# Kernel optimization log

Measured on AMD Instinct MI355X. Metric: run time of the kernel, lower is better.

The kernel has to match this reference:

```python
import jax, jax.numpy as jnp
import numpy as np

N = 50000      # nodes
E = 800000     # edges (before self-loops)
DIN = 2        # dim_input
DEMB = 128     # dim_embedding
H = 8          # n_heads
DV = 16        # dim_values (H*DV == DEMB)
DH = 512       # dim_hidden
L = 2          # n_att_layers
K = 10         # APPNP steps
ALPHA = 0.1
EPS = 1e-5     # BatchNorm eps
NEG_SLOPE = 0.2  # GAT leaky_relu slope


def setup_inputs() -> dict:
    key = jax.random.key(0)
    ks = jax.random.split(key, 16)
    s = 0.05
    inp = {}
    inp["x"] = jax.random.normal(ks[0], (N, DIN), jnp.float32)
    inp["J"] = jax.random.uniform(ks[1], (N, 1), jnp.float32)
    inp["edge_index"] = jax.random.randint(ks[2], (2, E), 0, N, jnp.int32)
    # Lin1: Linear(dim_input+1, dim_embedding)
    inp["lin0_w"] = jax.random.normal(ks[3], (DIN + 1, DEMB), jnp.float32) * s
    inp["lin0_b"] = jnp.zeros((DEMB,), jnp.float32)
    # Per attention layer (stacked over L):
    inp["gat_w"]   = jax.random.normal(ks[4], (L, DEMB, H * DV), jnp.float32) * s
    inp["att_src"] = jax.random.normal(ks[5], (L, H, DV), jnp.float32) * s
    inp["att_dst"] = jax.random.normal(ks[6], (L, H, DV), jnp.float32) * s
    inp["lin1_w"]  = jax.random.normal(ks[7], (L, DV, DEMB), jnp.float32) * s
    inp["bn1_g"]   = jnp.ones((L, DEMB), jnp.float32)
    inp["bn1_b"]   = jnp.zeros((L, DEMB), jnp.float32)
    inp["lin2_w"]  = jax.random.normal(ks[8], (L, DEMB, DH), jnp.float32) * s
    inp["lin2_b"]  = jnp.zeros((L, DH), jnp.float32)
    inp["lin3_w"]  = jax.random.normal(ks[9], (L, DH, DEMB), jnp.float32) * s
    inp["lin3_b"]  = jnp.zeros((L, DEMB), jnp.float32)
    inp["bn2_g"]   = jnp.ones((L, DEMB), jnp.float32)
    inp["bn2_b"]   = jnp.zeros((L, DEMB), jnp.float32)
    return inp


def _bn(z, g, b):
    # BatchNorm1d over nodes, training-mode batch statistics (biased var)
    mu = z.mean(0)
    var = jnp.mean((z - mu) ** 2, axis=0)
    return g * (z - mu) * jax.lax.rsqrt(var + EPS) + b


def reference(x, J, edge_index, lin0_w, lin0_b, gat_w, att_src, att_dst,
              lin1_w, bn1_g, bn1_b, lin2_w, lin2_b, lin3_w, lin3_b,
              bn2_g, bn2_b):
    # add self-loops (PyG GATConv and APPNP defaults)
    loop = jnp.arange(N, dtype=edge_index.dtype)
    src = jnp.concatenate([edge_index[0], loop])  # message source j
    dst = jnp.concatenate([edge_index[1], loop])  # message target i

    h = jnp.concatenate([x, J], axis=1) @ lin0_w + lin0_b  # [N, DEMB]

    for l in range(L):
        # ---- GATConv ----
        xl = (h @ gat_w[l]).reshape(N, H, DV)                # [N,H,DV]
        a_s = (xl * att_src[l]).sum(-1)                      # [N,H]
        a_d = (xl * att_dst[l]).sum(-1)                      # [N,H]
        e = jax.nn.leaky_relu(a_s[src] + a_d[dst], NEG_SLOPE)  # [E',H]
        e = e - jax.ops.segment_max(e, dst, num_segments=N)[dst]
        ee = jnp.exp(e)
        alpha = ee / jax.ops.segment_sum(ee, dst, num_segments=N)[dst]
        msg = xl[src] * alpha[:, :, None]                    # [E',H,DV]
        gat_out = jax.ops.segment_sum(msg, dst, num_segments=N)  # [N,H,DV]
        # lin1 per head then sum over heads
        hsum = jnp.einsum('nhc,cd->nd', gat_out, lin1_w[l])  # [N,DEMB]
        h1 = _bn(h + hsum, bn1_g[l], bn1_b[l])
        h2 = jax.nn.relu(h1 @ lin2_w[l] + lin2_b[l]) @ lin3_w[l] + lin3_b[l]
        h = _bn(h2 + h1, bn2_g[l], bn2_b[l])

    # ---- APPNP: K steps of (1-a)*Ahat h + a*h0, Ahat = D^-1/2 (A+I) D^-1/2 ----
    deg = jax.ops.segment_sum(jnp.ones_like(dst, jnp.float32), dst, num_segments=N)
    dinv = jax.lax.rsqrt(jnp.maximum(deg, 1.0))  # self-loops guarantee deg>=1
    norm = (dinv[src] * dinv[dst])[:, None]      # [E',1]
    h0 = h

    def step(hk, _):
        agg = jax.ops.segment_sum(norm * hk[src], dst, num_segments=N)
        return (1.0 - ALPHA) * agg + ALPHA * h0, None

    h, _ = jax.lax.scan(step, h, None, length=K)
    return jnp.concatenate([h, J], axis=1)  # [N, DEMB+1]
```

## Files before the change

kernel.cpp:

```cpp
#include <hip/hip_runtime.h>

#define NN 50000
#define NN1 50001
#define NP 50048
#define NMT64 782
#define NE 800000
#define EP (NE + NN)
#define EPP_MAX (EP + 7 * NN + 64)
#define DEMB 128
#define DHID 512
#define NB_SCAN 196

typedef unsigned short ushort_t;
typedef __attribute__((ext_vector_type(8))) short short8_t;
typedef __attribute__((ext_vector_type(4))) float float4_t;

__device__ __forceinline__ float bf2f(ushort_t u) {
    return __uint_as_float(((unsigned int)u) << 16);
}
__device__ __forceinline__ ushort_t f2bf(float f) {
    unsigned int x = __float_as_uint(f);
    x += 0x7fffu + ((x >> 16) & 1u);
    return (ushort_t)(x >> 16);
}
__device__ __forceinline__ float lo16(unsigned int w) { return __uint_as_float(w << 16); }
__device__ __forceinline__ float hi16(unsigned int w) { return __uint_as_float(w & 0xffff0000u); }
__device__ __forceinline__ unsigned int pack2(float a, float b) {
    return (unsigned int)f2bf(a) | ((unsigned int)f2bf(b) << 16);
}
__device__ __forceinline__ void gl_lds16(const ushort_t* g, ushort_t* l) {
    __builtin_amdgcn_global_load_lds(
        (const __attribute__((address_space(1))) void*)g,
        (__attribute__((address_space(3))) void*)l, 16, 0, 0);
}
static inline int cdiv(int a, int b) { return (a + b - 1) / b; }

__global__ void k_detect(const unsigned int* __restrict__ Jw, int* __restrict__ flag) {
    if (threadIdx.x != 0 || blockIdx.x != 0) return;
    int votes = 0;
    for (int i = 0; i < 8; ++i) {
        unsigned int w = Jw[i];
        unsigned int ex = (w >> 23) & 0xFFu;
        if ((w >> 31) == 0u && ex >= 100u && ex <= 126u) votes++;
    }
    *flag = (votes >= 6) ? 1 : 0;
}

struct CvtArgs {
    const void* src[16];
    float* dst[16];
    int n[16];
};
__global__ void k_cvt_all(CvtArgs a, const int* __restrict__ flag) {
    int which = blockIdx.y;
    int i = blockIdx.x * 256 + threadIdx.x;
    if (i >= a.n[which]) return;
    float v;
    if (*flag) v = ((const float*)a.src[which])[i];
    else       v = bf2f(((const ushort_t*)a.src[which])[i]);
    a.dst[which][i] = v;
}

struct TrArgs {
    const float* src[6];
    ushort_t* dst[6];
    int K[6];
    int Nc[6];
    int perm[6];
};
__global__ void k_tr_all(TrArgs a) {
    int which = blockIdx.y;
    int idx = blockIdx.x * 256 + threadIdx.x;
    int K = a.K[which], Nc = a.Nc[which];
    if (idx >= K * Nc) return;
    int k = idx / Nc, n = idx - k * Nc;
    int kd = k;
    if (a.perm[which]) {
        int kk = k & 63;
        kd = (k & ~63) | ((kk & 32) + 2 * (kk & 15) + ((kk >> 4) & 1));
    }
    a.dst[which][n * K + kd] = f2bf(a.src[which][idx]);
}

__global__ void k_deg(const int* __restrict__ ei, int* __restrict__ deg) {
    int e = blockIdx.x * 256 + threadIdx.x;
    if (e >= EP) return;
    int d = (e < NE) ? ei[NE + e] : (e - NE);
    atomicAdd(&deg[d], 1);
}

__global__ void k_part(const int* __restrict__ deg, int* __restrict__ part) {
    __shared__ int sm[256];
    int i = blockIdx.x * 256 + threadIdx.x;
    int v = (i < NN) ? deg[i] : 0;
    v = (v + 7) & ~7;
    sm[threadIdx.x] = v;
    __syncthreads();
    for (int off = 128; off > 0; off >>= 1) {
        if (threadIdx.x < off) sm[threadIdx.x] += sm[threadIdx.x + off];
        __syncthreads();
    }
    if (threadIdx.x == 0) part[blockIdx.x] = sm[0];
}

__global__ void k_scan2(const int* __restrict__ part, int* __restrict__ poff,
                        int* __restrict__ rowp) {
    __shared__ int sm[256];
    int t = threadIdx.x;
    int v = (t < NB_SCAN) ? part[t] : 0;
    sm[t] = v;
    __syncthreads();
    int incl = v;
    for (int off = 1; off < 256; off <<= 1) {
        int u = (t >= off) ? sm[t - off] : 0;
        __syncthreads();
        incl += u;
        sm[t] = incl;
        __syncthreads();
    }
    if (t < NB_SCAN) poff[t] = incl - v;
    if (t == 255) rowp[NN] = sm[255];
}

__global__ void k_rowp(const int* __restrict__ deg, const int* __restrict__ poff,
                       int* __restrict__ rowp, float* __restrict__ dinv,
                       int* __restrict__ fill) {
    __shared__ int sm[256];
    int i = blockIdx.x * 256 + threadIdx.x;
    int t = threadIdx.x;
    int rv = (i < NN) ? deg[i] : 0;
    int v = (rv + 7) & ~7;
    sm[t] = v;
    __syncthreads();
    int incl = v;
    for (int off = 1; off < 256; off <<= 1) {
        int u = (t >= off) ? sm[t - off] : 0;
        __syncthreads();
        incl += u;
        sm[t] = incl;
        __syncthreads();
    }
    if (i < NN) {
        int rp = poff[blockIdx.x] + incl - v;
        rowp[i] = rp;
        fill[i] = rp;
        dinv[i] = rsqrtf(fmaxf((float)rv, 1.0f));
    }
}

__global__ void k_fill(const int* __restrict__ ei, int* __restrict__ fillpos,
                       ushort_t* __restrict__ col) {
    int e = blockIdx.x * 256 + threadIdx.x;
    if (e >= EP) return;
    int s, d;
    if (e < NE) { s = ei[e]; d = ei[NE + e]; } else { s = d = e - NE; }
    int pos = atomicAdd(&fillpos[d], 1);
    col[pos] = (ushort_t)s;
}

__global__ void k_pad(const int* __restrict__ fillpos, const int* __restrict__ rowp,
                      ushort_t* __restrict__ col) {
    int n = blockIdx.x * 256 + threadIdx.x;
    if (n >= NN) return;
    int p = fillpos[n], p1 = rowp[n + 1];
    for (; p < p1; ++p) col[p] = (ushort_t)NN;
}

__global__ void k_zsent(unsigned int* __restrict__ a, unsigned int* __restrict__ b) {
    int t = threadIdx.x;
    if (t >= 64) return;
    int s = t >> 4, d = t & 15;
    size_t o = (size_t)s * NN1 * 16 + (size_t)NN * 16 + d;
    a[o] = 0;
    b[o] = 0;
}

__global__ void k_lin0(const float* __restrict__ x, const float* __restrict__ J,
                       const float* __restrict__ w, const float* __restrict__ b,
                       ushort_t* __restrict__ hB) {
    int idx = blockIdx.x * 256 + threadIdx.x;
    if (idx >= NN * DEMB) return;
    int n = idx >> 7, d = idx & 127;
    float v = x[n * 2] * w[d] + x[n * 2 + 1] * w[DEMB + d] + J[n] * w[2 * DEMB + d] + b[d];
    hB[idx] = f2bf(v);
}

__global__ void k_att(const unsigned int* __restrict__ xlB, const float* __restrict__ asrc,
                      const float* __restrict__ adst, float* __restrict__ a_s,
                      float* __restrict__ a_d) {
    int idx = blockIdx.x * 256 + threadIdx.x;
    if (idx >= NN * 8) return;
    int n = idx >> 3, hh = idx & 7;
    const unsigned int* row = xlB + (size_t)n * 64 + hh * 8;
    float s = 0.f, d = 0.f;
#pragma unroll
    for (int c = 0; c < 8; ++c) {
        unsigned int w = row[c];
        float v0 = lo16(w), v1 = hi16(w);
        s += v0 * asrc[hh * 16 + 2 * c] + v1 * asrc[hh * 16 + 2 * c + 1];
        d += v0 * adst[hh * 16 + 2 * c] + v1 * adst[hh * 16 + 2 * c + 1];
    }
    a_s[idx] = s;
    a_d[idx] = d;
}

__global__ __launch_bounds__(256) void k_z1s(const ushort_t* __restrict__ hB,
                                             const float* __restrict__ g,
                                             const float* __restrict__ w1,
                                             float* __restrict__ stats) {
    int d = threadIdx.x & 127;
    int rstart = blockIdx.x * 2 + (threadIdx.x >> 7);
    int stride = gridDim.x * 2;
    float s1 = 0.f, s2 = 0.f;
    for (int r = rstart; r < NN; r += stride) {
        const float* gr = g + r * 16;
        float s = bf2f(hB[(size_t)r * DEMB + d]);
#pragma unroll
        for (int c = 0; c < 16; ++c) s += gr[c] * w1[c * DEMB + d];
        s1 += s;
        s2 += s * s;
    }
    __shared__ float b1[256], b2[256];
    b1[threadIdx.x] = s1;
    b2[threadIdx.x] = s2;
    __syncthreads();
    if (threadIdx.x < 128) {
        atomicAdd(&stats[threadIdx.x], b1[threadIdx.x] + b1[threadIdx.x + 128]);
        atomicAdd(&stats[128 + threadIdx.x], b2[threadIdx.x] + b2[threadIdx.x + 128]);
    }
}

__global__ void k_bnapply1(const ushort_t* __restrict__ hB, const float* __restrict__ g,
                           const float* __restrict__ w1, const float* __restrict__ stats,
                           const float* __restrict__ gam, const float* __restrict__ bet,
                           ushort_t* __restrict__ outB) {
    int idx = blockIdx.x * 256 + threadIdx.x;
    if (idx >= NN * DEMB) return;
    int n = idx >> 7, d = idx & 127;
    float s = bf2f(hB[idx]);
    const float* gr = g + n * 16;
#pragma unroll
    for (int c = 0; c < 16; ++c) s += gr[c] * w1[c * DEMB + d];
    const float invN = 1.0f / (float)NN;
    float mu = stats[d] * invN;
    float var = stats[128 + d] * invN - mu * mu;
    float rs = rsqrtf(fmaxf(var, 0.f) + 1e-5f);
    float v = gam[d] * (s - mu) * rs + bet[d];
    outB[idx] = f2bf(v);
}

__global__ void k_bnapply(const ushort_t* __restrict__ zB, const float* __restrict__ stats,
                          const float* __restrict__ gam, const float* __restrict__ bet,
                          ushort_t* __restrict__ outB) {
    int idx = blockIdx.x * 256 + threadIdx.x;
    if (idx >= NN * DEMB) return;
    int d = idx & 127;
    const float invN = 1.0f / (float)NN;
    float mu = stats[d] * invN;
    float var = stats[128 + d] * invN - mu * mu;
    float rs = rsqrtf(fmaxf(var, 0.f) + 1e-5f);
    float v = gam[d] * (bf2f(zB[idx]) - mu) * rs + bet[d];
    outB[idx] = f2bf(v);
}

__global__ void k_bnapply_fin(const unsigned int* __restrict__ zB, const float* __restrict__ stats,
                              const float* __restrict__ gam, const float* __restrict__ bet,
                              const float* __restrict__ dinv,
                              unsigned int* __restrict__ hs, unsigned int* __restrict__ h0p) {
    int idx = blockIdx.x * 256 + threadIdx.x;
    if (idx >= NN * 64) return;
    int n = idx >> 6, j = idx & 63;
    int d0 = j * 2;
    const float invN = 1.0f / (float)NN;
    unsigned int zw = zB[idx];
    float z0 = lo16(zw), z1 = hi16(zw);
    float mu0 = stats[d0] * invN, mu1 = stats[d0 + 1] * invN;
    float v0 = stats[128 + d0] * invN - mu0 * mu0;
    float v1 = stats[128 + d0 + 1] * invN - mu1 * mu1;
    float rs0 = rsqrtf(fmaxf(v0, 0.f) + 1e-5f);
    float rs1 = rsqrtf(fmaxf(v1, 0.f) + 1e-5f);
    float a = gam[d0] * (z0 - mu0) * rs0 + bet[d0];
    float b = gam[d0 + 1] * (z1 - mu1) * rs1 + bet[d0 + 1];
    float di = dinv[n];
    int q = j >> 4, dd = j & 15;
    size_t o = (size_t)q * NN1 * 16 + (size_t)n * 16 + dd;
    hs[o] = pack2(di * a, di * b);
    h0p[o] = pack2(a, b);
}

__global__ __launch_bounds__(256) void k_gat(const int* __restrict__ rowp,
                                             const int* __restrict__ deg,
                                             const ushort_t* __restrict__ col,
                                             const float* __restrict__ a_s, const float* __restrict__ a_d,
                                             const unsigned int* __restrict__ xlB, float* __restrict__ g) {
    int wid = (blockIdx.x * 256 + threadIdx.x) >> 6;
    int lane = threadIdx.x & 63;
    if (wid >= NN) return;
    int p0 = rowp[wid], p1 = p0 + deg[wid];
    int hh = lane >> 3;
    float ad2 = a_d[wid * 8 + hh];
    float acc0 = 0.f, acc1 = 0.f, s = 0.f;
    int p = p0;
    while (p < p1) {
        int cnt = p1 - p;
        if (cnt > 64) cnt = 64;
        int pl = p + lane;
        int jv = (int)col[pl < p1 ? pl : (p1 - 1)];
        int i = 0;
        for (; i + 8 <= cnt; i += 8) {
            int j0 = __shfl(jv, i),     j1 = __shfl(jv, i + 1);
            int j2 = __shfl(jv, i + 2), j3 = __shfl(jv, i + 3);
            int j4 = __shfl(jv, i + 4), j5 = __shfl(jv, i + 5);
            int j6 = __shfl(jv, i + 6), j7 = __shfl(jv, i + 7);
            float e0 = a_s[j0 * 8 + hh] + ad2, e1 = a_s[j1 * 8 + hh] + ad2;
            float e2 = a_s[j2 * 8 + hh] + ad2, e3 = a_s[j3 * 8 + hh] + ad2;
            float e4 = a_s[j4 * 8 + hh] + ad2, e5 = a_s[j5 * 8 + hh] + ad2;
            float e6 = a_s[j6 * 8 + hh] + ad2, e7 = a_s[j7 * 8 + hh] + ad2;
            unsigned int w0 = xlB[j0 * 64 + lane], w1 = xlB[j1 * 64 + lane];
            unsigned int w2 = xlB[j2 * 64 + lane], w3 = xlB[j3 * 64 + lane];
            unsigned int w4 = xlB[j4 * 64 + lane], w5 = xlB[j5 * 64 + lane];
            unsigned int w6 = xlB[j6 * 64 + lane], w7 = xlB[j7 * 64 + lane];
            e0 = e0 > 0.f ? e0 : 0.2f * e0;  e1 = e1 > 0.f ? e1 : 0.2f * e1;
            e2 = e2 > 0.f ? e2 : 0.2f * e2;  e3 = e3 > 0.f ? e3 : 0.2f * e3;
            e4 = e4 > 0.f ? e4 : 0.2f * e4;  e5 = e5 > 0.f ? e5 : 0.2f * e5;
            e6 = e6 > 0.f ? e6 : 0.2f * e6;  e7 = e7 > 0.f ? e7 : 0.2f * e7;
            float al0 = __expf(e0), al1 = __expf(e1), al2 = __expf(e2), al3 = __expf(e3);
            float al4 = __expf(e4), al5 = __expf(e5), al6 = __expf(e6), al7 = __expf(e7);
            s += al0 + al1 + al2 + al3 + al4 + al5 + al6 + al7;
            acc0 += al0 * lo16(w0) + al1 * lo16(w1) + al2 * lo16(w2) + al3 * lo16(w3) +
                    al4 * lo16(w4) + al5 * lo16(w5) + al6 * lo16(w6) + al7 * lo16(w7);
            acc1 += al0 * hi16(w0) + al1 * hi16(w1) + al2 * hi16(w2) + al3 * hi16(w3) +
                    al4 * hi16(w4) + al5 * hi16(w5) + al6 * hi16(w6) + al7 * hi16(w7);
        }
        for (; i < cnt; ++i) {
            int j = __shfl(jv, i);
            float e = a_s[j * 8 + hh] + ad2;
            e = e > 0.f ? e : 0.2f * e;
            float al = __expf(e);
            unsigned int w = xlB[j * 64 + lane];
            s += al;
            acc0 += al * lo16(w);
            acc1 += al * hi16(w);
        }
        p += cnt;
    }
    float inv = 1.f / s;
    acc0 *= inv;
    acc1 *= inv;
    acc0 += __shfl_xor(acc0, 8);  acc1 += __shfl_xor(acc1, 8);
    acc0 += __shfl_xor(acc0, 16); acc1 += __shfl_xor(acc1, 16);
    acc0 += __shfl_xor(acc0, 32); acc1 += __shfl_xor(acc1, 32);
    if (lane < 8) ((float2*)g)[wid * 8 + lane] = make_float2(acc0, acc1);
}

__global__ __launch_bounds__(256) void k_appnp(const int* __restrict__ rowp,
                                               const ushort_t* __restrict__ col,
                                               const float* __restrict__ dinv,
                                               const unsigned int* __restrict__ hs,
                                               const unsigned int* __restrict__ h0p,
                                               unsigned int* __restrict__ hs_out,
                                               const float* __restrict__ Jf,
                                               const int* __restrict__ flag,
                                               void* __restrict__ out, int writeOut) {
    int b = blockIdx.x;
    int w = threadIdx.x >> 6, lane = threadIdx.x & 63;
    int s = (b & 7) >> 1;
    int g = ((b >> 3) << 1) + (b & 1);
    int ns = lane >> 4, d = lane & 15;
    int n = g * 16 + w * 4 + ns;
    int valid = (n < NN);
    int nc = valid ? n : (NN - 1);
    int p0 = rowp[nc], p1 = rowp[nc + 1];
    const unsigned int* hsq = hs + (size_t)s * NN1 * 16;
    unsigned int hw = h0p[(size_t)s * NN1 * 16 + (size_t)nc * 16 + d];
    float di = dinv[nc];
    int base = ns << 4;
    float a0 = 0.f, a1 = 0.f;
    int p = p0;
    while (p < p1) {
        int rem = p1 - p;
        int jv = (int)col[p + d];
        {
            int j0 = __shfl(jv, base + 0), j1 = __shfl(jv, base + 1);
            int j2 = __shfl(jv, base + 2), j3 = __shfl(jv, base + 3);
            int j4 = __shfl(jv, base + 4), j5 = __shfl(jv, base + 5);
            int j6 = __shfl(jv, base + 6), j7 = __shfl(jv, base + 7);
            unsigned int w0 = hsq[j0 * 16 + d], w1 = hsq[j1 * 16 + d];
            unsigned int w2 = hsq[j2 * 16 + d], w3 = hsq[j3 * 16 + d];
            unsigned int w4 = hsq[j4 * 16 + d], w5 = hsq[j5 * 16 + d];
            unsigned int w6 = hsq[j6 * 16 + d], w7 = hsq[j7 * 16 + d];
            a0 += lo16(w0) + lo16(w1) + lo16(w2) + lo16(w3) +
                  lo16(w4) + lo16(w5) + lo16(w6) + lo16(w7);
            a1 += hi16(w0) + hi16(w1) + hi16(w2) + hi16(w3) +
                  hi16(w4) + hi16(w5) + hi16(w6) + hi16(w7);
        }
        if (rem > 8) {
            int j0 = __shfl(jv, base + 8),  j1 = __shfl(jv, base + 9);
            int j2 = __shfl(jv, base + 10), j3 = __shfl(jv, base + 11);
            int j4 = __shfl(jv, base + 12), j5 = __shfl(jv, base + 13);
            int j6 = __shfl(jv, base + 14), j7 = __shfl(jv, base + 15);
            unsigned int w0 = hsq[j0 * 16 + d], w1 = hsq[j1 * 16 + d];
            unsigned int w2 = hsq[j2 * 16 + d], w3 = hsq[j3 * 16 + d];
            unsigned int w4 = hsq[j4 * 16 + d], w5 = hsq[j5 * 16 + d];
            unsigned int w6 = hsq[j6 * 16 + d], w7 = hsq[j7 * 16 + d];
            a0 += lo16(w0) + lo16(w1) + lo16(w2) + lo16(w3) +
                  lo16(w4) + lo16(w5) + lo16(w6) + lo16(w7);
            a1 += hi16(w0) + hi16(w1) + hi16(w2) + hi16(w3) +
                  hi16(w4) + hi16(w5) + hi16(w6) + hi16(w7);
        }
        p += 16;
    }
    float n0 = 0.9f * di * a0 + 0.1f * lo16(hw);
    float n1 = 0.9f * di * a1 + 0.1f * hi16(hw);
    if (valid) {
        if (!writeOut) {
            hs_out[(size_t)s * NN1 * 16 + (size_t)n * 16 + d] = pack2(di * n0, di * n1);
        } else {
            size_t obase = (size_t)n * 129 + s * 32 + 2 * d;
            if (*flag) {
                float* o = (float*)out;
                o[obase] = n0;
                o[obase + 1] = n1;
                if (s == 0 && d == 0) o[(size_t)n * 129 + 128] = Jf[n];
            } else {
                ushort_t* o = (ushort_t*)out;
                o[obase] = f2bf(n0);
                o[obase + 1] = f2bf(n1);
                if (s == 0 && d == 0) o[(size_t)n * 129 + 128] = f2bf(Jf[n]);
            }
        }
    }
}

template <int MODE>
__global__ __launch_bounds__(256) void k_gemm64(const ushort_t* __restrict__ A,
                                                const ushort_t* __restrict__ Bt,
                                                int M, int K, int Nc,
                                                const float* __restrict__ bias,
                                                const ushort_t* __restrict__ res,
                                                ushort_t* __restrict__ outB,
                                                float* __restrict__ stats) {
    __shared__ __align__(16) ushort_t lsA[2][64 * 32];
    __shared__ __align__(16) ushort_t lsB[2][128 * 32];
    int t = threadIdx.x;
    int m0 = blockIdx.x * 64;
    int n0 = blockIdx.y * 128;
    int w = t >> 6, lane = t & 63;
    int row16 = lane & 15, quad = lane >> 4;
    int nbase = w * 32;
    float4_t acc[8];
#pragma unroll
    for (int i = 0; i < 8; ++i) acc[i] = (float4_t){0.f, 0.f, 0.f, 0.f};
    int lrow = lane >> 2;
    int lcol = (lane & 3) * 8;
    const ushort_t* gA  = A  + (size_t)(m0 + w * 16 + lrow) * K + lcol;
    const ushort_t* gB0 = Bt + (size_t)(n0 + w * 32 + lrow) * K + lcol;
    const ushort_t* gB1 = Bt + (size_t)(n0 + w * 32 + 16 + lrow) * K + lcol;
    ushort_t* dA  = &lsA[0][0] + (w * 16) * 32;
    ushort_t* dB0 = &lsB[0][0] + (w * 32) * 32;
    ushort_t* dB1 = &lsB[0][0] + (w * 32 + 16) * 32;
    const int bufStrideA = 64 * 32, bufStrideB = 128 * 32;
    const int nK = K >> 5;
    gl_lds16(gA, dA);
    gl_lds16(gB0, dB0);
    gl_lds16(gB1, dB1);
    for (int kb = 0; kb < nK; ++kb) {
        __syncthreads();
        int nb = kb + 1;
        if (nb < nK) {
            int b = nb & 1;
            int k0 = nb << 5;
            gl_lds16(gA + k0, dA + b * bufStrideA);
            gl_lds16(gB0 + k0, dB0 + b * bufStrideB);
            gl_lds16(gB1 + k0, dB1 + b * bufStrideB);
        }
        const ushort_t* la = &lsA[kb & 1][0];
        const ushort_t* lb = &lsB[kb & 1][0];
        short8_t afr[4], bfr[2];
#pragma unroll
        for (int i = 0; i < 4; ++i)
            afr[i] = *(const short8_t*)(la + (i * 16 + row16) * 32 + quad * 8);
#pragma unroll
        for (int i = 0; i < 2; ++i)
            bfr[i] = *(const short8_t*)(lb + (nbase + i * 16 + row16) * 32 + quad * 8);
#pragma unroll
        for (int mt = 0; mt < 4; ++mt)
#pragma unroll
            for (int nt = 0; nt < 2; ++nt)
                acc[mt * 2 + nt] = __builtin_amdgcn_mfma_f32_16x16x32_bf16(
                    afr[mt], bfr[nt], acc[mt * 2 + nt], 0, 0, 0);
    }
#pragma unroll
    for (int mt = 0; mt < 4; ++mt) {
#pragma unroll
        for (int nt = 0; nt < 2; ++nt) {
            int cc = n0 + nbase + nt * 16 + row16;
#pragma unroll
            for (int r = 0; r < 4; ++r) {
                int rr = m0 + mt * 16 + quad * 4 + r;
                if (rr < M) {
                    outB[(size_t)rr * Nc + cc] = f2bf(acc[mt * 2 + nt][r]);
                }
            }
        }
    }
}

__global__ __launch_bounds__(256, 3) void k_ffn(const ushort_t* __restrict__ A,
                                                const ushort_t* __restrict__ W2t,
                                                const ushort_t* __restrict__ W3t,
                                                const float* __restrict__ b2,
                                                const float* __restrict__ b3,
                                                const ushort_t* __restrict__ res,
                                                ushort_t* __restrict__ outB,
                                                float* __restrict__ stats) {
    __shared__ __align__(16) ushort_t sW2[4 * 64 * 32];
    __shared__ __align__(16) ushort_t sW3[2 * 128 * 32];
    __shared__ __align__(16) ushort_t sAH[4 * 2048];
    int t = threadIdx.x;
    int w = t >> 6, lane = t & 63;
    int wm = w >> 1, wn = w & 1;
    int m0 = blockIdx.x * 64;
    int row16 = lane & 15, quad = lane >> 4;
    int sw = (row16 >> 2) & 3;
    int srow = lane >> 2;
    int klin = lane & 3;

#pragma unroll
    for (int i = 0; i < 4; ++i) {
        int row = i * 16 + srow;
        int kc = klin ^ ((row >> 2) & 3);
        gl_lds16(A + (size_t)(m0 + row) * 128 + w * 32 + kc * 8,
                 sAH + w * 2048 + i * 512);
        gl_lds16(W2t + (size_t)row * 128 + w * 32 + kc * 8,
                 sW2 + w * 2048 + i * 512);
        int f = w * 4 + i;
        int ks = f >> 3;
        int n3 = (f & 7) * 16 + srow;
        int kc3 = klin ^ ((n3 >> 2) & 3);
        gl_lds16(W3t + (size_t)n3 * 512 + ks * 32 + kc3 * 8,
                 sW3 + f * 512);
    }
    __syncthreads();

    short8_t afrA[2][4];
#pragma unroll
    for (int mt = 0; mt < 2; ++mt)
#pragma unroll
        for (int kb = 0; kb < 4; ++kb)
            afrA[mt][kb] = *(const short8_t*)(sAH + kb * 2048 +
                                              (wm * 32 + mt * 16 + row16) * 32 + (quad ^ sw) * 8);
    __syncthreads();

    char* Hb = (char*)sAH;
    float* s1 = (float*)(Hb + 8192);
    float* s2 = s1 + 128;
    if (t < 128) { s1[t] = 0.f; s2[t] = 0.f; }

    float4_t accz[2][4];
#pragma unroll
    for (int mt = 0; mt < 2; ++mt)
#pragma unroll
        for (int nt = 0; nt < 4; ++nt) accz[mt][nt] = (float4_t){0.f, 0.f, 0.f, 0.f};

    for (int c = 0; c < 8; ++c) {
        float b20 = b2[c * 64 + wn * 32 + row16];
        float b21 = b2[c * 64 + wn * 32 + 16 + row16];
        float4_t acch[2][2];
#pragma unroll
        for (int mt = 0; mt < 2; ++mt)
#pragma unroll
            for (int nt = 0; nt < 2; ++nt) acch[mt][nt] = (float4_t){0.f, 0.f, 0.f, 0.f};
#pragma unroll
        for (int kb = 0; kb < 4; ++kb) {
            short8_t b0 = *(const short8_t*)(sW2 + kb * 2048 +
                                             (wn * 32 + row16) * 32 + (quad ^ sw) * 8);
            short8_t b1 = *(const short8_t*)(sW2 + kb * 2048 +
                                             (wn * 32 + 16 + row16) * 32 + (quad ^ sw) * 8);
            acch[0][0] = __builtin_amdgcn_mfma_f32_16x16x32_bf16(afrA[0][kb], b0, acch[0][0], 0, 0, 0);
            acch[0][1] = __builtin_amdgcn_mfma_f32_16x16x32_bf16(afrA[0][kb], b1, acch[0][1], 0, 0, 0);
            acch[1][0] = __builtin_amdgcn_mfma_f32_16x16x32_bf16(afrA[1][kb], b0, acch[1][0], 0, 0, 0);
            acch[1][1] = __builtin_amdgcn_mfma_f32_16x16x32_bf16(afrA[1][kb], b1, acch[1][1], 0, 0, 0);
        }
#pragma unroll
        for (int mt = 0; mt < 2; ++mt) {
#pragma unroll
            for (int r = 0; r < 4; ++r) {
                int row = wm * 32 + mt * 16 + quad * 4 + r;
                int d = wn * 16 + row16;
                int byteOff = row * 128 + ((((d >> 2) ^ (row & 7))) << 4) + (d & 3) * 4;
                float v0 = acch[mt][0][r] + b20; v0 = v0 > 0.f ? v0 : 0.f;
                float v1 = acch[mt][1][r] + b21; v1 = v1 > 0.f ? v1 : 0.f;
                *(unsigned int*)(Hb + byteOff) = pack2(v0, v1);
            }
        }
        __syncthreads();
        if (c < 7) {
#pragma unroll
            for (int i = 0; i < 4; ++i) {
                int n = i * 16 + srow;
                int kc = klin ^ ((n >> 2) & 3);
                gl_lds16(W2t + (size_t)((c + 1) * 64 + n) * 128 + w * 32 + kc * 8,
                         sW2 + w * 2048 + i * 512);
            }
        }
#pragma unroll
        for (int ks = 0; ks < 2; ++ks) {
            short8_t afrH[2];
#pragma unroll
            for (int mt = 0; mt < 2; ++mt)
                afrH[mt] = *(const short8_t*)(Hb + (wm * 32 + mt * 16 + row16) * 128 +
                                              (((ks * 4 + quad) ^ (row16 & 7)) << 4));
#pragma unroll
            for (int nt = 0; nt < 4; ++nt) {
                short8_t bfr = *(const short8_t*)(sW3 + ks * 4096 +
                                                  (wn * 64 + nt * 16 + row16) * 32 + (quad ^ sw) * 8);
                accz[0][nt] = __builtin_amdgcn_mfma_f32_16x16x32_bf16(afrH[0], bfr, accz[0][nt], 0, 0, 0);
                accz[1][nt] = __builtin_amdgcn_mfma_f32_16x16x32_bf16(afrH[1], bfr, accz[1][nt], 0, 0, 0);
            }
        }
        __syncthreads();
        if (c < 7) {
#pragma unroll
            for (int i = 0; i < 4; ++i) {
                int f = w * 4 + i;
                int ks = f >> 3;
                int n = (f & 7) * 16 + srow;
                int kc = klin ^ ((n >> 2) & 3);
                gl_lds16(W3t + (size_t)n * 512 + (c + 1) * 64 + ks * 32 + kc * 8,
                         sW3 + f * 512);
            }
        }
    }

#pragma unroll
    for (int mt = 0; mt < 2; ++mt) {
#pragma unroll
        for (int nt = 0; nt < 4; ++nt) {
            int cc = wn * 64 + nt * 16 + row16;
            float bv = b3[cc];
            float ls = 0.f, lq = 0.f;
#pragma unroll
            for (int r = 0; r < 4; ++r) {
                int rr = m0 + wm * 32 + mt * 16 + quad * 4 + r;
                if (rr < NN) {
                    float v = accz[mt][nt][r] + bv + bf2f(res[(size_t)rr * 128 + cc]);
                    outB[(size_t)rr * 128 + cc] = f2bf(v);
                    ls += v;
                    lq += v * v;
                }
            }
            atomicAdd(&s1[cc], ls);
            atomicAdd(&s2[cc], lq);
        }
    }
    __syncthreads();
    if (t < 128) {
        atomicAdd(&stats[t], s1[t]);
        atomicAdd(&stats[128 + t], s2[t]);
    }
}

extern "C" void kernel_launch(void* const* d_in, const int* in_sizes, int n_in,
                              void* d_out, int out_size, void* d_ws, size_t ws_size,
                              hipStream_t stream) {
    const int* ei = (const int*)d_in[2];

    char* p = (char*)d_ws;
    auto alloc = [&](size_t bytes) {
        void* r = (void*)p;
        p += (bytes + 255) & ~(size_t)255;
        return r;
    };
    ushort_t* hB    = (ushort_t*)alloc((size_t)NP * DEMB * 2);
    ushort_t* h1B   = (ushort_t*)alloc((size_t)NP * DEMB * 2);
    ushort_t* xlB   = (ushort_t*)alloc((size_t)NN * DEMB * 2);
    unsigned int* hsA  = (unsigned int*)alloc((size_t)4 * NN1 * 16 * 4);
    unsigned int* hsB_ = (unsigned int*)alloc((size_t)4 * NN1 * 16 * 4);
    unsigned int* h0p  = (unsigned int*)alloc((size_t)4 * NN1 * 16 * 4);
    float*    asv   = (float*)alloc((size_t)NN * 8 * 4);
    float*    adv   = (float*)alloc((size_t)NN * 8 * 4);
    float*    gv    = (float*)alloc((size_t)NN * 16 * 4);
    float*    dinvv = (float*)alloc((size_t)NN * 4);
    float*    stats = (float*)alloc(4 * 256 * 4);
    int*      deg   = (int*)alloc((size_t)NN * 4);
    int*      rowp  = (int*)alloc((size_t)(NN + 1) * 4);
    int*      fill  = (int*)alloc((size_t)NN * 4);
    ushort_t* colv  = (ushort_t*)alloc((size_t)EPP_MAX * 2);
    int*      part  = (int*)alloc(NB_SCAN * 4);
    int*      poff  = (int*)alloc(NB_SCAN * 4);
    int*      flag  = (int*)alloc(256);
    ushort_t* wtg   = (ushort_t*)alloc((size_t)2 * 128 * 128 * 2);
    ushort_t* wt2   = (ushort_t*)alloc((size_t)2 * 512 * 128 * 2);
    ushort_t* wt3   = (ushort_t*)alloc((size_t)2 * 128 * 512 * 2);
    float* xf   = (float*)alloc((size_t)NN * 2 * 4);
    float* Jf   = (float*)alloc((size_t)NN * 4);
    float* l0wF = (float*)alloc(384 * 4);
    float* l0bF = (float*)alloc(128 * 4);
    float* gwF  = (float*)alloc(32768 * 4);
    float* asF  = (float*)alloc(256 * 4);
    float* adF  = (float*)alloc(256 * 4);
    float* w1F  = (float*)alloc(4096 * 4);
    float* b1gF = (float*)alloc(256 * 4);
    float* b1bF = (float*)alloc(256 * 4);
    float* w2F  = (float*)alloc(131072 * 4);
    float* b2F  = (float*)alloc(1024 * 4);
    float* w3F  = (float*)alloc(131072 * 4);
    float* b3F  = (float*)alloc(256 * 4);
    float* b2gF = (float*)alloc(256 * 4);
    float* b2bF = (float*)alloc(256 * 4);

    k_detect<<<1, 64, 0, stream>>>((const unsigned int*)d_in[1], flag);
    CvtArgs ca;
    {
        const int srcIdx[16] = {0, 1, 3, 4, 5, 6, 7, 8, 9, 10, 11, 12, 13, 14, 15, 16};
        float* dsts[16] = {xf, Jf, l0wF, l0bF, gwF, asF, adF, w1F, b1gF, b1bF,
                           w2F, b2F, w3F, b3F, b2gF, b2bF};
        const int ns[16] = {NN * 2, NN, 384, 128, 32768, 256, 256, 4096, 256, 256,
                            131072, 1024, 131072, 256, 256, 256};
        for (int i = 0; i < 16; ++i) { ca.src[i] = d_in[srcIdx[i]]; ca.dst[i] = dsts[i]; ca.n[i] = ns[i]; }
    }
    k_cvt_all<<<dim3(cdiv(131072, 256), 16), 256, 0, stream>>>(ca, flag);

    hipMemsetAsync(deg, 0, (size_t)NN * 4, stream);
    hipMemsetAsync(stats, 0, 4 * 256 * 4, stream);
    k_deg<<<cdiv(EP, 256), 256, 0, stream>>>(ei, deg);
    k_part<<<NB_SCAN, 256, 0, stream>>>(deg, part);
    k_scan2<<<1, 256, 0, stream>>>(part, poff, rowp);
    k_rowp<<<NB_SCAN, 256, 0, stream>>>(deg, poff, rowp, dinvv, fill);
    k_fill<<<cdiv(EP, 256), 256, 0, stream>>>(ei, fill, colv);
    k_pad<<<cdiv(NN, 256), 256, 0, stream>>>(fill, rowp, colv);
    k_zsent<<<1, 64, 0, stream>>>(hsA, hsB_);

    TrArgs ta;
    {
        const float* srcs[6] = {gwF, gwF + 16384, w2F, w2F + 65536, w3F, w3F + 65536};
        ushort_t* dsts[6] = {wtg, wtg + 16384, wt2, wt2 + 65536, wt3, wt3 + 65536};
        const int Ks[6] = {128, 128, 128, 128, 512, 512};
        const int Ncs[6] = {128, 128, 512, 512, 128, 128};
        const int perms[6] = {0, 0, 0, 0, 1, 1};
        for (int i = 0; i < 6; ++i) {
            ta.src[i] = srcs[i]; ta.dst[i] = dsts[i]; ta.K[i] = Ks[i]; ta.Nc[i] = Ncs[i];
            ta.perm[i] = perms[i];
        }
    }
    k_tr_all<<<dim3(cdiv(65536, 256), 6), 256, 0, stream>>>(ta);

    k_lin0<<<cdiv(NN * DEMB, 256), 256, 0, stream>>>(xf, Jf, l0wF, l0bF, hB);

    for (int l = 0; l < 2; ++l) {
        float* st1 = stats + (l * 2 + 0) * 256;
        float* st2 = stats + (l * 2 + 1) * 256;
        ushort_t* zB = xlB;
        k_gemm64<3><<<dim3(NMT64, 1), 256, 0, stream>>>(hB, wtg + l * 16384, NN, 128, 128,
                                                        nullptr, nullptr, xlB, nullptr);
        k_att<<<cdiv(NN * 8, 256), 256, 0, stream>>>((const unsigned int*)xlB, asF + l * 128,
                                                     adF + l * 128, asv, adv);
        k_gat<<<cdiv(NN * 64, 256), 256, 0, stream>>>(rowp, deg, colv, asv, adv,
                                                      (const unsigned int*)xlB, gv);
        k_z1s<<<512, 256, 0, stream>>>(hB, gv, w1F + l * 2048, st1);
        k_bnapply1<<<cdiv(NN * DEMB, 256), 256, 0, stream>>>(hB, gv, w1F + l * 2048, st1,
                                                             b1gF + l * 128, b1bF + l * 128,
                                                             h1B);
        k_ffn<<<NMT64, 256, 0, stream>>>(h1B, wt2 + l * 65536, wt3 + l * 65536,
                                         b2F + l * 512, b3F + l * 128, h1B, zB, st2);
        if (l == 0) {
            k_bnapply<<<cdiv(NN * DEMB, 256), 256, 0, stream>>>(zB, st2, b2gF, b2bF, hB);
        } else {
            k_bnapply_fin<<<cdiv(NN * 64, 256), 256, 0, stream>>>((const unsigned int*)zB, st2,
                                                                  b2gF + 128, b2bF + 128,
                                                                  dinvv, hsA, h0p);
        }
    }

    unsigned int* pin = hsA;
    unsigned int* pout = hsB_;
    for (int k = 0; k < 10; ++k) {
        int last = (k == 9) ? 1 : 0;
        k_appnp<<<12504, 256, 0, stream>>>(rowp, colv, dinvv, pin, h0p, pout,
                                           Jf, flag, d_out, last);
        unsigned int* tmp = pout;
        pout = pin;
        pin = tmp;
    }
}
```

Measured before the change: 823.4 us.

## Widen APPNP gathers to 8-byte loads with two edge subgroups and 16-padding

The APPNP propagation kernel now has each lane load a uint2 (four bf16 features) per neighbor instead of a single uint. Each 16-lane group is split into two 8-lane halves that process alternating edges, and the halves are combined with a shuffle-xor at the end. CSR row padding grows from multiples of 8 to multiples of 16, so the branch for partial chunks is removed. The intent is fewer, wider memory transactions on the irregular gather and less control flow, at the cost of more padded dummy edges and an extra cross-lane reduction.

```diff
diff --git a/kernel.cpp b/kernel.cpp
--- a/kernel.cpp
+++ b/kernel.cpp
@@ -6,7 +6,7 @@
 #define NMT64 782
 #define NE 800000
 #define EP (NE + NN)
-#define EPP_MAX (EP + 7 * NN + 64)
+#define EPP_MAX (EP + 15 * NN + 64)
 #define DEMB 128
 #define DHID 512
 #define NB_SCAN 196
@@ -93,7 +93,7 @@
     __shared__ int sm[256];
     int i = blockIdx.x * 256 + threadIdx.x;
     int v = (i < NN) ? deg[i] : 0;
-    v = (v + 7) & ~7;
+    v = (v + 15) & ~15;
     sm[threadIdx.x] = v;
     __syncthreads();
     for (int off = 128; off > 0; off >>= 1) {
@@ -129,7 +129,7 @@
     int i = blockIdx.x * 256 + threadIdx.x;
     int t = threadIdx.x;
     int rv = (i < NN) ? deg[i] : 0;
-    int v = (rv + 7) & ~7;
+    int v = (rv + 15) & ~15;
     sm[t] = v;
     __syncthreads();
     int incl = v;
@@ -366,67 +366,65 @@
     int w = threadIdx.x >> 6, lane = threadIdx.x & 63;
     int s = (b & 7) >> 1;
     int g = ((b >> 3) << 1) + (b & 1);
-    int ns = lane >> 4, d = lane & 15;
+    int ns = lane >> 4, gl = lane & 15;
+    int dp = gl & 7, es = gl >> 3;
     int n = g * 16 + w * 4 + ns;
     int valid = (n < NN);
     int nc = valid ? n : (NN - 1);
     int p0 = rowp[nc], p1 = rowp[nc + 1];
-    const unsigned int* hsq = hs + (size_t)s * NN1 * 16;
-    unsigned int hw = h0p[(size_t)s * NN1 * 16 + (size_t)nc * 16 + d];
+    const uint2* hsq = (const uint2*)(hs + (size_t)s * NN1 * 16);
+    uint2 hw = ((const uint2*)(h0p + (size_t)s * NN1 * 16))[(size_t)nc * 8 + dp];
     float di = dinv[nc];
-    int base = ns << 4;
-    float a0 = 0.f, a1 = 0.f;
-    int p = p0;
-    while (p < p1) {
-        int rem = p1 - p;
-        int jv = (int)col[p + d];
-        {
-            int j0 = __shfl(jv, base + 0), j1 = __shfl(jv, base + 1);
-            int j2 = __shfl(jv, base + 2), j3 = __shfl(jv, base + 3);
-            int j4 = __shfl(jv, base + 4), j5 = __shfl(jv, base + 5);
-            int j6 = __shfl(jv, base + 6), j7 = __shfl(jv, base + 7);
-            unsigned int w0 = hsq[j0 * 16 + d], w1 = hsq[j1 * 16 + d];
-            unsigned int w2 = hsq[j2 * 16 + d], w3 = hsq[j3 * 16 + d];
-            unsigned int w4 = hsq[j4 * 16 + d], w5 = hsq[j5 * 16 + d];
-            unsigned int w6 = hsq[j6 * 16 + d], w7 = hsq[j7 * 16 + d];
-            a0 += lo16(w0) + lo16(w1) + lo16(w2) + lo16(w3) +
-                  lo16(w4) + lo16(w5) + lo16(w6) + lo16(w7);
-            a1 += hi16(w0) + hi16(w1) + hi16(w2) + hi16(w3) +
-                  hi16(w4) + hi16(w5) + hi16(w6) + hi16(w7);
-        }
-        if (rem > 8) {
-            int j0 = __shfl(jv, base + 8),  j1 = __shfl(jv, base + 9);
-            int j2 = __shfl(jv, base + 10), j3 = __shfl(jv, base + 11);
-            int j4 = __shfl(jv, base + 12), j5 = __shfl(jv, base + 13);
-            int j6 = __shfl(jv, base + 14), j7 = __shfl(jv, base + 15);
-            unsigned int w0 = hsq[j0 * 16 + d], w1 = hsq[j1 * 16 + d];
-            unsigned int w2 = hsq[j2 * 16 + d], w3 = hsq[j3 * 16 + d];
-            unsigned int w4 = hsq[j4 * 16 + d], w5 = hsq[j5 * 16 + d];
-            unsigned int w6 = hsq[j6 * 16 + d], w7 = hsq[j7 * 16 + d];
-            a0 += lo16(w0) + lo16(w1) + lo16(w2) + lo16(w3) +
-                  lo16(w4) + lo16(w5) + lo16(w6) + lo16(w7);
-            a1 += hi16(w0) + hi16(w1) + hi16(w2) + hi16(w3) +
-                  hi16(w4) + hi16(w5) + hi16(w6) + hi16(w7);
-        }
-        p += 16;
-    }
-    float n0 = 0.9f * di * a0 + 0.1f * lo16(hw);
-    float n1 = 0.9f * di * a1 + 0.1f * hi16(hw);
-    if (valid) {
+    int base = (ns << 4) + es;
+    float a0 = 0.f, a1 = 0.f, a2 = 0.f, a3 = 0.f;
+    for (int p = p0; p < p1; p += 16) {
+        int jv = (int)col[p + gl];
+        int j0 = __shfl(jv, base + 0),  j1 = __shfl(jv, base + 2);
+        int j2 = __shfl(jv, base + 4),  j3 = __shfl(jv, base + 6);
+        int j4 = __shfl(jv, base + 8),  j5 = __shfl(jv, base + 10);
+        int j6 = __shfl(jv, base + 12), j7 = __shfl(jv, base + 14);
+        uint2 w0 = hsq[(size_t)j0 * 8 + dp], w1 = hsq[(size_t)j1 * 8 + dp];
+        uint2 w2 = hsq[(size_t)j2 * 8 + dp], w3 = hsq[(size_t)j3 * 8 + dp];
+        uint2 w4 = hsq[(size_t)j4 * 8 + dp], w5 = hsq[(size_t)j5 * 8 + dp];
+        uint2 w6 = hsq[(size_t)j6 * 8 + dp], w7 = hsq[(size_t)j7 * 8 + dp];
+        a0 += lo16(w0.x) + lo16(w1.x) + lo16(w2.x) + lo16(w3.x) +
+              lo16(w4.x) + lo16(w5.x) + lo16(w6.x) + lo16(w7.x);
+        a1 += hi16(w0.x) + hi16(w1.x) + hi16(w2.x) + hi16(w3.x) +
+              hi16(w4.x) + hi16(w5.x) + hi16(w6.x) + hi16(w7.x);
+        a2 += lo16(w0.y) + lo16(w1.y) + lo16(w2.y) + lo16(w3.y) +
+              lo16(w4.y) + lo16(w5.y) + lo16(w6.y) + lo16(w7.y);
+        a3 += hi16(w0.y) + hi16(w1.y) + hi16(w2.y) + hi16(w3.y) +
+              hi16(w4.y) + hi16(w5.y) + hi16(w6.y) + hi16(w7.y);
+    }
+    a0 += __shfl_xor(a0, 8);
+    a1 += __shfl_xor(a1, 8);
+    a2 += __shfl_xor(a2, 8);
+    a3 += __shfl_xor(a3, 8);
+    float n0 = 0.9f * di * a0 + 0.1f * lo16(hw.x);
+    float n1 = 0.9f * di * a1 + 0.1f * hi16(hw.x);
+    float n2 = 0.9f * di * a2 + 0.1f * lo16(hw.y);
+    float n3 = 0.9f * di * a3 + 0.1f * hi16(hw.y);
+    if (valid && es == 0) {
         if (!writeOut) {
-            hs_out[(size_t)s * NN1 * 16 + (size_t)n * 16 + d] = pack2(di * n0, di * n1);
+            uint2* o2 = (uint2*)(hs_out + (size_t)s * NN1 * 16);
+            o2[(size_t)n * 8 + dp] = make_uint2(pack2(di * n0, di * n1),
+                                                pack2(di * n2, di * n3));
         } else {
-            size_t obase = (size_t)n * 129 + s * 32 + 2 * d;
+            size_t obase = (size_t)n * 129 + s * 32 + 4 * dp;
             if (*flag) {
                 float* o = (float*)out;
                 o[obase] = n0;
                 o[obase + 1] = n1;
-                if (s == 0 && d == 0) o[(size_t)n * 129 + 128] = Jf[n];
+                o[obase + 2] = n2;
+                o[obase + 3] = n3;
+                if (s == 0 && dp == 0) o[(size_t)n * 129 + 128] = Jf[n];
             } else {
                 ushort_t* o = (ushort_t*)out;
                 o[obase] = f2bf(n0);
                 o[obase + 1] = f2bf(n1);
-                if (s == 0 && d == 0) o[(size_t)n * 129 + 128] = f2bf(Jf[n]);
+                o[obase + 2] = f2bf(n2);
+                o[obase + 3] = f2bf(n3);
+                if (s == 0 && dp == 0) o[(size_t)n * 129 + 128] = f2bf(Jf[n]);
             }
         }
     }
```

Result: slower. 898.9 us (+9.2%).
